# Kernel optimization log

Measured on AMD Instinct MI355X. Metric: run time of the kernel, lower is better.

The kernel has to match this reference:

```python
import jax, jax.numpy as jnp
import numpy as np

BIG = 1.0e6  # cost for empty groups
EPS = 1e-6

COST_ACTIVITY = 1.0
COST_GROUP = 1.0
COST_SIZE = 1.0


def setup_inputs() -> dict:
    key = jax.random.key(0)
    k1, k2, k3, k4 = jax.random.split(key, 4)
    bs, Q, C = 256, 512, 128   # batch, num_queries, num_activity_classes
    P, G = 256, 128            # num_persons, num_target_groups
    return {
        "pred_activity_logits": jax.random.normal(k1, (bs, Q, C), dtype=jnp.float32),
        "attention_logits": jax.random.normal(k2, (bs, P, Q), dtype=jnp.float32),
        "tgt_activity_ids": jax.random.randint(k3, (bs, G), 0, C),
        "tgt_group_ids": jax.random.randint(k4, (bs, P), 0, G),
    }


def reference(pred_activity_logits, attention_logits, tgt_activity_ids, tgt_group_ids):
    bs, Q, C = pred_activity_logits.shape
    P = attention_logits.shape[1]
    G = tgt_activity_ids.shape[1]

    # out_attw_b.T -> [Q, P]; log_softmax over dim 0 (queries)
    attw = jnp.transpose(attention_logits, (0, 2, 1))          # [bs, Q, P]
    logP = jax.nn.log_softmax(attw, axis=1)                    # softmax over queries
    P_qn = jnp.exp(logP)
    P_clamped = jnp.clip(P_qn, EPS, 1.0 - EPS)
    lognegP = jnp.log1p(-P_clamped)                            # [bs, Q, P]

    # one-hot grouping target: M[b, p, g] = 1 iff person p in group g
    M = jax.nn.one_hot(tgt_group_ids, G, dtype=logP.dtype)     # [bs, P, G]
    m = M.sum(axis=1)                                          # [bs, G] members per group
    nm = P - m                                                 # nonmembers per group

    # grouping cost: -mean member logP - mean nonmember log(1-P)
    mem_sum = jnp.einsum('bqp,bpg->bqg', logP, M)
    non_sum = jnp.einsum('bqp,bpg->bqg', lognegP, 1.0 - M)
    safe_m = jnp.maximum(m, 1.0)[:, None, :]
    safe_nm = jnp.maximum(nm, 1.0)[:, None, :]
    grouping_cost = -mem_sum / safe_m - non_sum / safe_nm      # [bs, Q, G]

    # size cost: |sum_p P_qn - m| / n_person
    pred_size = P_qn.sum(axis=2)                               # [bs, Q]
    size_cost = jnp.abs(pred_size[:, :, None] - m[:, None, :]) / max(float(P), 1.0)

    empty = (m == 0)[:, None, :]                               # [bs, 1, G]
    grouping_cost = jnp.where(empty, BIG, grouping_cost)
    size_cost = jnp.where(empty, BIG, size_cost)

    # activity cost: cross-entropy of query logits vs each group's activity class
    logq = jax.nn.log_softmax(pred_activity_logits, axis=-1)   # [bs, Q, C]
    idx = jnp.broadcast_to(tgt_activity_ids[:, None, :], (bs, Q, G))
    activity_cost = -jnp.take_along_axis(logq, idx, axis=2)    # [bs, Q, G]

    cost = (COST_GROUP * grouping_cost
            + COST_ACTIVITY * activity_cost
            + COST_SIZE * size_cost)
    return cost
```

## Files before the change

### kernel.cpp

```cpp
#include <hip/hip_runtime.h>

#define BS 256
#define NQ 512
#define NC 128
#define NP 256
#define NG 128
#define TQ 32
#define PTS (NC + 1)
#define BIGC 1.0e6f
#define EPSC 1e-6f


__global__ __launch_bounds__(512, 8) void lse_kernel(const float* __restrict__ att,
                                                     float* __restrict__ lse) {
    const int t   = threadIdx.x;
    const int wv  = t >> 6, ln = t & 63;
    const int row = blockIdx.x * 8 + wv;
    const float4* a4 = (const float4*)(att + (size_t)row * NQ);
    const float4 v0 = a4[2 * ln];
    const float4 v1 = a4[2 * ln + 1];

    float mx = fmaxf(fmaxf(fmaxf(v0.x, v0.y), fmaxf(v0.z, v0.w)),
                     fmaxf(fmaxf(v1.x, v1.y), fmaxf(v1.z, v1.w)));
#pragma unroll
    for (int off = 1; off < 64; off <<= 1) mx = fmaxf(mx, __shfl_xor(mx, off, 64));

    float s = __expf(v0.x - mx) + __expf(v0.y - mx) + __expf(v0.z - mx) + __expf(v0.w - mx)
            + __expf(v1.x - mx) + __expf(v1.y - mx) + __expf(v1.z - mx) + __expf(v1.w - mx);
#pragma unroll
    for (int off = 1; off < 64; off <<= 1) s += __shfl_xor(s, off, 64);

    if (ln == 0) lse[row] = mx + __logf(s);
}

__global__ __launch_bounds__(512, 8) void cost_kernel(
    const float* __restrict__ predAct,
    const float* __restrict__ att,
    const int*   __restrict__ actIds,
    const int*   __restrict__ grpIds,
    const float* __restrict__ lseAtt,
    float*       __restrict__ out)
{
    __shared__ float wS[(NP + 1) * TQ];
    __shared__ float scratch[512];
    __shared__ float redS[512];
    __shared__ float lseAct[TQ];
    __shared__ float szG[TQ], slG[TQ];
    __shared__ int   aidS[NG];
    __shared__ int   cntS[NG];

    float* lseS  = scratch;
    int*   prS   = (int*)(scratch + 256);
    float* scanP = scratch;
    float* pTile = wS;

    const int b  = blockIdx.x >> 4;
    const int q0 = (blockIdx.x & 15) * TQ;
    const int t  = threadIdx.x;

    const int pr  = t >> 3;
    const int qo4 = (t & 7) * 4;
    float4 v[4];
#pragma unroll
    for (int it = 0; it < 4; ++it)
        v[it] = *(const float4*)(att + ((size_t)(b * NP + it * 64 + pr)) * NQ + q0 + qo4);

    const int wv = t >> 6, ln = t & 63;
    float pa0[4], pa1[4];
#pragma unroll
    for (int k = 0; k < 4; ++k) {
        const float* rowp = predAct + ((size_t)(b * NQ + q0 + wv + 8 * k)) * NC;
        pa0[k] = rowp[ln]; pa1[k] = rowp[ln + 64];
    }

    if (t < NP) { lseS[t] = lseAtt[b * NP + t]; prS[t] = grpIds[b * NP + t]; }
    if (t < NG) { aidS[t] = actIds[b * NG + t]; cntS[t] = 0; }
    __syncthreads();

    int myPos = 0;
    if (t < NP) myPos = atomicAdd(&cntS[prS[t]], 1);
    __syncthreads();

    if (t < 64) {
        const int c0 = cntS[2 * t], c1 = cntS[2 * t + 1];
        const int ps = c0 + c1;
        int s = ps;
#pragma unroll
        for (int off = 1; off < 64; off <<= 1) {
            const int w = __shfl_up(s, off, 64);
            if (t >= off) s += w;
        }
        const int e = s - ps;
        cntS[2 * t]     = e | (c0 << 16);
        cntS[2 * t + 1] = (e + c0) | (c1 << 16);
    }
    __syncthreads();
    if (t < NP) {
        const int g  = prS[t];
        const int cs = cntS[g];
        prS[t] = ((cs & 0xffff) + myPos) | (cs & 0xffff0000);
    }
    __syncthreads();

    float szL[4] = {0.f, 0.f, 0.f, 0.f}, slL[4] = {0.f, 0.f, 0.f, 0.f};
#pragma unroll
    for (int it = 0; it < 4; ++it) {
        const int p  = it * 64 + pr;
        const float l = lseS[p];
        const int pk = prS[p];
        const int rr = pk & 0xffff;
        const int m  = pk >> 16;
        const float im  = 1.f / (float)m;
        const float inm = 1.f / fmaxf((float)(NP - m), 1.f);
        float w[4];
        const float vv[4] = {v[it].x, v[it].y, v[it].z, v[it].w};
#pragma unroll
        for (int j = 0; j < 4; ++j) {
            const float x = vv[j] - l;
            const float e = __expf(x);
            const float c = fminf(fmaxf(e, EPSC), 1.f - EPSC);
            const float ll = __logf(1.f - c);
            szL[j] += e;
            slL[j] += ll;
            w[j] = ll * inm - x * im;
        }
        *(float4*)(wS + rr * TQ + qo4) = *(float4*)w;
    }
#pragma unroll
    for (int j = 0; j < 4; ++j) {
#pragma unroll
        for (int off = 8; off < 64; off <<= 1) {
            szL[j] += __shfl_xor(szL[j], off, 64);
            slL[j] += __shfl_xor(slL[j], off, 64);
        }
    }
    if (ln < 8) {
        *(float4*)(redS + wv * 32 + ln * 4)       = *(float4*)szL;
        *(float4*)(redS + 256 + wv * 32 + ln * 4) = *(float4*)slL;
    }

#pragma unroll
    for (int k = 0; k < 4; ++k) {
        const int r = wv + 8 * k;
        float mx = fmaxf(pa0[k], pa1[k]);
#pragma unroll
        for (int off = 1; off < 64; off <<= 1) mx = fmaxf(mx, __shfl_xor(mx, off, 64));
        float s = __expf(pa0[k] - mx) + __expf(pa1[k] - mx);
#pragma unroll
        for (int off = 1; off < 64; off <<= 1) s += __shfl_xor(s, off, 64);
        if (ln == 0) lseAct[r] = mx + __logf(s);
    }
    __syncthreads();

    if (t < 64) {
        const int q = t & 31, which = t >> 5;
        const float* rb = redS + which * 256 + q;
        float s = 0.f;
#pragma unroll
        for (int w8 = 0; w8 < 8; ++w8) s += rb[w8 * 32];
        if (which == 0) szG[q] = s; else slG[q] = s;
    }

    {
        const int cq = t & 31;
        const int ck = t >> 5;
        float pv[16];
        float run = 0.f;
#pragma unroll
        for (int i = 0; i < 16; ++i) {
            pv[i] = run;
            run += wS[(16 * ck + i) * TQ + cq];
        }
        scanP[ck * 32 + cq] = run;
        __syncthreads();
        float offs = 0.f;
#pragma unroll
        for (int j = 0; j < 15; ++j)
            if (j < ck) offs += scanP[j * 32 + cq];
#pragma unroll
        for (int i = 0; i < 16; ++i)
            wS[(16 * ck + i) * TQ + cq] = offs + pv[i];
        if (ck == 15) wS[NP * TQ + cq] = offs + run;
    }
    __syncthreads();

    const int qoC = t & 31;
    const int g4A = (t >> 5) * 4;
    const int g4B = g4A + 64;
    float resA[4], resB[4];
    {
        const float sl = slG[qoC], pz = szG[qoC];
#pragma unroll
        for (int rep = 0; rep < 2; ++rep) {
            float* res = rep ? resB : resA;
            const int g4 = rep ? g4B : g4A;
#pragma unroll
            for (int j = 0; j < 4; ++j) {
                const int g  = g4 + j;
                const int cs = cntS[g];
                const int m  = cs >> 16;
                const int st = cs & 0xffff;
                const float ms = wS[(st + m) * TQ + qoC] - wS[st * TQ + qoC];
                const float mf  = (float)m;
                const float nmf = fmaxf((float)(NP - m), 1.f);
                float grp = ms - sl / nmf;
                float szc = fabsf(pz - mf) * (1.f / (float)NP);
                if (m == 0) { grp = BIGC; szc = BIGC; }
                res[j] = grp + szc;
            }
        }
    }
    __syncthreads();

#pragma unroll
    for (int k = 0; k < 4; ++k) {
        const int r = wv + 8 * k;
        pTile[r * PTS + ln]      = pa0[k];
        pTile[r * PTS + 64 + ln] = pa1[k];
    }
    __syncthreads();

    {
        const float la = lseAct[qoC];
#pragma unroll
        for (int rep = 0; rep < 2; ++rep) {
            float* res = rep ? resB : resA;
            const int g4 = rep ? g4B : g4A;
#pragma unroll
            for (int j = 0; j < 4; ++j) {
                const float av = pTile[qoC * PTS + aidS[g4 + j]];
                res[j] += la - av;
            }
            *(float4*)(out + ((size_t)(b * NQ + q0 + qoC)) * NG + g4) = *(float4*)res;
        }
    }
}

extern "C" void kernel_launch(void* const* d_in, const int* in_sizes, int n_in,
                              void* d_out, int out_size, void* d_ws, size_t ws_size,
                              hipStream_t stream) {
    const float* predAct = (const float*)d_in[0];
    const float* att     = (const float*)d_in[1];
    const int*   actIds  = (const int*)d_in[2];
    const int*   grpIds  = (const int*)d_in[3];
    float*       out     = (float*)d_out;
    float*       lse     = (float*)d_ws;

    lse_kernel<<<(BS * NP) / 8, 512, 0, stream>>>(att, lse);
    cost_kernel<<<BS * (NQ / TQ), 512, 0, stream>>>(predAct, att, actIds, grpIds, lse, out);
}
```

Before: 282.9 us.

## Fuse LSE pass into cost kernel with per-batch persistent blocks

Removes the separate attention log-sum-exp kernel and its workspace round-trip. Each block now handles half a batch, computes the LSE for all persons itself, then loops over eight query tiles. This saves a launch and the LSE write/read. In exchange, the attention LSE work is duplicated across the two blocks per batch, and the grid shrinks to 512 blocks with serialized tiles, which reduces parallelism and latency hiding.

```diff
diff --git a/kernel.cpp b/kernel.cpp
--- a/kernel.cpp
+++ b/kernel.cpp
@@ -10,70 +10,61 @@
 #define BIGC 1.0e6f
 #define EPSC 1e-6f
 
-
-__global__ __launch_bounds__(512, 8) void lse_kernel(const float* __restrict__ att,
-                                                     float* __restrict__ lse) {
-    const int t   = threadIdx.x;
-    const int wv  = t >> 6, ln = t & 63;
-    const int row = blockIdx.x * 8 + wv;
-    const float4* a4 = (const float4*)(att + (size_t)row * NQ);
-    const float4 v0 = a4[2 * ln];
-    const float4 v1 = a4[2 * ln + 1];
-
-    float mx = fmaxf(fmaxf(fmaxf(v0.x, v0.y), fmaxf(v0.z, v0.w)),
-                     fmaxf(fmaxf(v1.x, v1.y), fmaxf(v1.z, v1.w)));
-#pragma unroll
-    for (int off = 1; off < 64; off <<= 1) mx = fmaxf(mx, __shfl_xor(mx, off, 64));
-
-    float s = __expf(v0.x - mx) + __expf(v0.y - mx) + __expf(v0.z - mx) + __expf(v0.w - mx)
-            + __expf(v1.x - mx) + __expf(v1.y - mx) + __expf(v1.z - mx) + __expf(v1.w - mx);
-#pragma unroll
-    for (int off = 1; off < 64; off <<= 1) s += __shfl_xor(s, off, 64);
-
-    if (ln == 0) lse[row] = mx + __logf(s);
-}
-
-__global__ __launch_bounds__(512, 8) void cost_kernel(
+__global__ __launch_bounds__(512, 4) void cost_fused(
     const float* __restrict__ predAct,
     const float* __restrict__ att,
     const int*   __restrict__ actIds,
     const int*   __restrict__ grpIds,
-    const float* __restrict__ lseAtt,
     float*       __restrict__ out)
 {
     __shared__ float wS[(NP + 1) * TQ];
-    __shared__ float scratch[512];
+    __shared__ float scanP[512];
     __shared__ float redS[512];
+    __shared__ float lseS[NP];
+    __shared__ int   prS[NP];
     __shared__ float lseAct[TQ];
     __shared__ float szG[TQ], slG[TQ];
     __shared__ int   aidS[NG];
     __shared__ int   cntS[NG];
 
-    float* lseS  = scratch;
-    int*   prS   = (int*)(scratch + 256);
-    float* scanP = scratch;
     float* pTile = wS;
 
-    const int b  = blockIdx.x >> 4;
-    const int q0 = (blockIdx.x & 15) * TQ;
-    const int t  = threadIdx.x;
-
+    const int b   = blockIdx.x >> 1;
+    const int qh  = (blockIdx.x & 1) * 256;
+    const int t   = threadIdx.x;
+    const int wv  = t >> 6, ln = t & 63;
     const int pr  = t >> 3;
     const int qo4 = (t & 7) * 4;
-    float4 v[4];
-#pragma unroll
-    for (int it = 0; it < 4; ++it)
-        v[it] = *(const float4*)(att + ((size_t)(b * NP + it * 64 + pr)) * NQ + q0 + qo4);
-
-    const int wv = t >> 6, ln = t & 63;
-    float pa0[4], pa1[4];
-#pragma unroll
-    for (int k = 0; k < 4; ++k) {
-        const float* rowp = predAct + ((size_t)(b * NQ + q0 + wv + 8 * k)) * NC;
-        pa0[k] = rowp[ln]; pa1[k] = rowp[ln + 64];
-    }
-
-    if (t < NP) { lseS[t] = lseAtt[b * NP + t]; prS[t] = grpIds[b * NP + t]; }
+
+    {
+        const float* base = att + (size_t)b * NP * NQ;
+#pragma unroll
+        for (int bt = 0; bt < 8; ++bt) {
+            const int r0 = wv * 32 + bt * 4;
+            float4 u0[4], u1[4];
+#pragma unroll
+            for (int i = 0; i < 4; ++i) {
+                const float4* a4 = (const float4*)(base + (size_t)(r0 + i) * NQ);
+                u0[i] = a4[2 * ln]; u1[i] = a4[2 * ln + 1];
+            }
+#pragma unroll
+            for (int i = 0; i < 4; ++i) {
+                float mx = fmaxf(fmaxf(fmaxf(u0[i].x, u0[i].y), fmaxf(u0[i].z, u0[i].w)),
+                                 fmaxf(fmaxf(u1[i].x, u1[i].y), fmaxf(u1[i].z, u1[i].w)));
+#pragma unroll
+                for (int off = 1; off < 64; off <<= 1) mx = fmaxf(mx, __shfl_xor(mx, off, 64));
+                float s = __expf(u0[i].x - mx) + __expf(u0[i].y - mx)
+                        + __expf(u0[i].z - mx) + __expf(u0[i].w - mx)
+                        + __expf(u1[i].x - mx) + __expf(u1[i].y - mx)
+                        + __expf(u1[i].z - mx) + __expf(u1[i].w - mx);
+#pragma unroll
+                for (int off = 1; off < 64; off <<= 1) s += __shfl_xor(s, off, 64);
+                if (ln == 0) lseS[r0 + i] = mx + __logf(s);
+            }
+        }
+    }
+
+    if (t < NP) prS[t] = grpIds[b * NP + t];
     if (t < NG) { aidS[t] = actIds[b * NG + t]; cntS[t] = 0; }
     __syncthreads();
 
@@ -102,137 +93,154 @@
     }
     __syncthreads();
 
-    float szL[4] = {0.f, 0.f, 0.f, 0.f}, slL[4] = {0.f, 0.f, 0.f, 0.f};
-#pragma unroll
-    for (int it = 0; it < 4; ++it) {
-        const int p  = it * 64 + pr;
-        const float l = lseS[p];
-        const int pk = prS[p];
-        const int rr = pk & 0xffff;
-        const int m  = pk >> 16;
-        const float im  = 1.f / (float)m;
-        const float inm = 1.f / fmaxf((float)(NP - m), 1.f);
-        float w[4];
-        const float vv[4] = {v[it].x, v[it].y, v[it].z, v[it].w};
+    for (int tt = 0; tt < 8; ++tt) {
+        const int q0 = qh + tt * TQ;
+
+        float4 v[4];
+#pragma unroll
+        for (int it = 0; it < 4; ++it)
+            v[it] = *(const float4*)(att + ((size_t)(b * NP + it * 64 + pr)) * NQ + q0 + qo4);
+
+        float pa0[4], pa1[4];
+#pragma unroll
+        for (int k = 0; k < 4; ++k) {
+            const float* rowp = predAct + ((size_t)(b * NQ + q0 + wv + 8 * k)) * NC;
+            pa0[k] = rowp[ln]; pa1[k] = rowp[ln + 64];
+        }
+
+        float szL[4] = {0.f, 0.f, 0.f, 0.f}, slL[4] = {0.f, 0.f, 0.f, 0.f};
+#pragma unroll
+        for (int it = 0; it < 4; ++it) {
+            const int p  = it * 64 + pr;
+            const float l = lseS[p];
+            const int pk = prS[p];
+            const int rr = pk & 0xffff;
+            const int m  = pk >> 16;
+            const float im  = 1.f / (float)m;
+            const float inm = 1.f / fmaxf((float)(NP - m), 1.f);
+            float w[4];
+            const float vv[4] = {v[it].x, v[it].y, v[it].z, v[it].w};
+#pragma unroll
+            for (int j = 0; j < 4; ++j) {
+                const float x = vv[j] - l;
+                const float e = __expf(x);
+                const float c = fminf(fmaxf(e, EPSC), 1.f - EPSC);
+                const float ll = __logf(1.f - c);
+                szL[j] += e;
+                slL[j] += ll;
+                w[j] = ll * inm - x * im;
+            }
+            *(float4*)(wS + rr * TQ + qo4) = *(float4*)w;
+        }
 #pragma unroll
         for (int j = 0; j < 4; ++j) {
-            const float x = vv[j] - l;
-            const float e = __expf(x);
-            const float c = fminf(fmaxf(e, EPSC), 1.f - EPSC);
-            const float ll = __logf(1.f - c);
-            szL[j] += e;
-            slL[j] += ll;
-            w[j] = ll * inm - x * im;
-        }
-        *(float4*)(wS + rr * TQ + qo4) = *(float4*)w;
-    }
-#pragma unroll
-    for (int j = 0; j < 4; ++j) {
-#pragma unroll
-        for (int off = 8; off < 64; off <<= 1) {
-            szL[j] += __shfl_xor(szL[j], off, 64);
-            slL[j] += __shfl_xor(slL[j], off, 64);
-        }
-    }
-    if (ln < 8) {
-        *(float4*)(redS + wv * 32 + ln * 4)       = *(float4*)szL;
-        *(float4*)(redS + 256 + wv * 32 + ln * 4) = *(float4*)slL;
-    }
-
-#pragma unroll
-    for (int k = 0; k < 4; ++k) {
-        const int r = wv + 8 * k;
-        float mx = fmaxf(pa0[k], pa1[k]);
-#pragma unroll
-        for (int off = 1; off < 64; off <<= 1) mx = fmaxf(mx, __shfl_xor(mx, off, 64));
-        float s = __expf(pa0[k] - mx) + __expf(pa1[k] - mx);
-#pragma unroll
-        for (int off = 1; off < 64; off <<= 1) s += __shfl_xor(s, off, 64);
-        if (ln == 0) lseAct[r] = mx + __logf(s);
-    }
-    __syncthreads();
-
-    if (t < 64) {
-        const int q = t & 31, which = t >> 5;
-        const float* rb = redS + which * 256 + q;
-        float s = 0.f;
-#pragma unroll
-        for (int w8 = 0; w8 < 8; ++w8) s += rb[w8 * 32];
-        if (which == 0) szG[q] = s; else slG[q] = s;
-    }
-
-    {
-        const int cq = t & 31;
-        const int ck = t >> 5;
-        float pv[16];
-        float run = 0.f;
-#pragma unroll
-        for (int i = 0; i < 16; ++i) {
-            pv[i] = run;
-            run += wS[(16 * ck + i) * TQ + cq];
-        }
-        scanP[ck * 32 + cq] = run;
-        __syncthreads();
-        float offs = 0.f;
-#pragma unroll
-        for (int j = 0; j < 15; ++j)
-            if (j < ck) offs += scanP[j * 32 + cq];
-#pragma unroll
-        for (int i = 0; i < 16; ++i)
-            wS[(16 * ck + i) * TQ + cq] = offs + pv[i];
-        if (ck == 15) wS[NP * TQ + cq] = offs + run;
-    }
-    __syncthreads();
-
-    const int qoC = t & 31;
-    const int g4A = (t >> 5) * 4;
-    const int g4B = g4A + 64;
-    float resA[4], resB[4];
-    {
-        const float sl = slG[qoC], pz = szG[qoC];
-#pragma unroll
-        for (int rep = 0; rep < 2; ++rep) {
-            float* res = rep ? resB : resA;
-            const int g4 = rep ? g4B : g4A;
-#pragma unroll
-            for (int j = 0; j < 4; ++j) {
-                const int g  = g4 + j;
-                const int cs = cntS[g];
-                const int m  = cs >> 16;
-                const int st = cs & 0xffff;
-                const float ms = wS[(st + m) * TQ + qoC] - wS[st * TQ + qoC];
-                const float mf  = (float)m;
-                const float nmf = fmaxf((float)(NP - m), 1.f);
-                float grp = ms - sl / nmf;
-                float szc = fabsf(pz - mf) * (1.f / (float)NP);
-                if (m == 0) { grp = BIGC; szc = BIGC; }
-                res[j] = grp + szc;
-            }
-        }
-    }
-    __syncthreads();
-
-#pragma unroll
-    for (int k = 0; k < 4; ++k) {
-        const int r = wv + 8 * k;
-        pTile[r * PTS + ln]      = pa0[k];
-        pTile[r * PTS + 64 + ln] = pa1[k];
-    }
-    __syncthreads();
-
-    {
-        const float la = lseAct[qoC];
-#pragma unroll
-        for (int rep = 0; rep < 2; ++rep) {
-            float* res = rep ? resB : resA;
-            const int g4 = rep ? g4B : g4A;
-#pragma unroll
-            for (int j = 0; j < 4; ++j) {
-                const float av = pTile[qoC * PTS + aidS[g4 + j]];
-                res[j] += la - av;
-            }
-            *(float4*)(out + ((size_t)(b * NQ + q0 + qoC)) * NG + g4) = *(float4*)res;
-        }
+#pragma unroll
+            for (int off = 8; off < 64; off <<= 1) {
+                szL[j] += __shfl_xor(szL[j], off, 64);
+                slL[j] += __shfl_xor(slL[j], off, 64);
+            }
+        }
+        if (ln < 8) {
+            *(float4*)(redS + wv * 32 + ln * 4)       = *(float4*)szL;
+            *(float4*)(redS + 256 + wv * 32 + ln * 4) = *(float4*)slL;
+        }
+
+#pragma unroll
+        for (int k = 0; k < 4; ++k) {
+            const int r = wv + 8 * k;
+            float mx = fmaxf(pa0[k], pa1[k]);
+#pragma unroll
+            for (int off = 1; off < 64; off <<= 1) mx = fmaxf(mx, __shfl_xor(mx, off, 64));
+            float s = __expf(pa0[k] - mx) + __expf(pa1[k] - mx);
+#pragma unroll
+            for (int off = 1; off < 64; off <<= 1) s += __shfl_xor(s, off, 64);
+            if (ln == 0) lseAct[r] = mx + __logf(s);
+        }
+        __syncthreads();
+
+        if (t < 64) {
+            const int q = t & 31, which = t >> 5;
+            const float* rb = redS + which * 256 + q;
+            float s = 0.f;
+#pragma unroll
+            for (int w8 = 0; w8 < 8; ++w8) s += rb[w8 * 32];
+            if (which == 0) szG[q] = s; else slG[q] = s;
+        }
+
+        {
+            const int cq = t & 31;
+            const int ck = t >> 5;
+            float pv[16];
+            float run = 0.f;
+#pragma unroll
+            for (int i = 0; i < 16; ++i) {
+                pv[i] = run;
+                run += wS[(16 * ck + i) * TQ + cq];
+            }
+            scanP[ck * 32 + cq] = run;
+            __syncthreads();
+            float offs = 0.f;
+#pragma unroll
+            for (int j = 0; j < 15; ++j)
+                if (j < ck) offs += scanP[j * 32 + cq];
+#pragma unroll
+            for (int i = 0; i < 16; ++i)
+                wS[(16 * ck + i) * TQ + cq] = offs + pv[i];
+            if (ck == 15) wS[NP * TQ + cq] = offs + run;
+        }
+        __syncthreads();
+
+        const int qoC = t & 31;
+        const int g4A = (t >> 5) * 4;
+        const int g4B = g4A + 64;
+        float resA[4], resB[4];
+        {
+            const float sl = slG[qoC], pz = szG[qoC];
+#pragma unroll
+            for (int rep = 0; rep < 2; ++rep) {
+                float* res = rep ? resB : resA;
+                const int g4 = rep ? g4B : g4A;
+#pragma unroll
+                for (int j = 0; j < 4; ++j) {
+                    const int g  = g4 + j;
+                    const int cs = cntS[g];
+                    const int m  = cs >> 16;
+                    const int st = cs & 0xffff;
+                    const float ms = wS[(st + m) * TQ + qoC] - wS[st * TQ + qoC];
+                    const float mf  = (float)m;
+                    const float nmf = fmaxf((float)(NP - m), 1.f);
+                    float grp = ms - sl / nmf;
+                    float szc = fabsf(pz - mf) * (1.f / (float)NP);
+                    if (m == 0) { grp = BIGC; szc = BIGC; }
+                    res[j] = grp + szc;
+                }
+            }
+        }
+        __syncthreads();
+
+#pragma unroll
+        for (int k = 0; k < 4; ++k) {
+            const int r = wv + 8 * k;
+            pTile[r * PTS + ln]      = pa0[k];
+            pTile[r * PTS + 64 + ln] = pa1[k];
+        }
+        __syncthreads();
+
+        {
+            const float la = lseAct[qoC];
+#pragma unroll
+            for (int rep = 0; rep < 2; ++rep) {
+                float* res = rep ? resB : resA;
+                const int g4 = rep ? g4B : g4A;
+#pragma unroll
+                for (int j = 0; j < 4; ++j) {
+                    const float av = pTile[qoC * PTS + aidS[g4 + j]];
+                    res[j] += la - av;
+                }
+                *(float4*)(out + ((size_t)(b * NQ + q0 + qoC)) * NG + g4) = *(float4*)res;
+            }
+        }
+        __syncthreads();
     }
 }
 
@@ -244,8 +252,7 @@
     const int*   actIds  = (const int*)d_in[2];
     const int*   grpIds  = (const int*)d_in[3];
     float*       out     = (float*)d_out;
-    float*       lse     = (float*)d_ws;
-
-    lse_kernel<<<(BS * NP) / 8, 512, 0, stream>>>(att, lse);
-    cost_kernel<<<BS * (NQ / TQ), 512, 0, stream>>>(predAct, att, actIds, grpIds, lse, out);
+    (void)d_ws; (void)ws_size;
+
+    cost_fused<<<BS * 2, 512, 0, stream>>>(predAct, att, actIds, grpIds, out);
 }
```

New measurement: 311.5 us. 10.1% more time.
